# Kernel tuning notes

Hardware: AMD Instinct MI355X
Metric: run time of the kernel (lower is better)

The kernel has to match this reference:

```python
import jax, jax.numpy as jnp
import numpy as np


def _lstm_layer(x, w_ih, w_hh, b_ih, b_hh):
    """Single PyTorch-style LSTM layer (gate order i,f,g,o). x: [B,T,D] -> [B,T,H]."""
    B, T, _ = x.shape
    H = w_hh.shape[1]
    # Precompute input projections for all timesteps (one big GEMM).
    xp = jnp.einsum('btd,gd->btg', x, w_ih) + b_ih + b_hh  # [B,T,4H]

    def step(carry, xt):
        h, c = carry
        gates = xt + h @ w_hh.T  # [B,4H]
        i, f, g, o = jnp.split(gates, 4, axis=-1)
        i = jax.nn.sigmoid(i)
        f = jax.nn.sigmoid(f)
        g = jnp.tanh(g)
        o = jax.nn.sigmoid(o)
        c = f * c + i * g
        h = o * jnp.tanh(c)
        return (h, c), h

    init = (jnp.zeros((B, H), x.dtype), jnp.zeros((B, H), x.dtype))
    _, hs = jax.lax.scan(step, init, jnp.swapaxes(xp, 0, 1))  # hs: [T,B,H]
    return jnp.swapaxes(hs, 0, 1)


def setup_inputs() -> dict:
    key = jax.random.key(0)
    ks = jax.random.split(key, 11)
    B, T, D, H, O = 256, 512, 64, 512, 1
    s_in = 1.0 / np.sqrt(H)
    inp = {
        'x': jax.random.normal(ks[0], (B, T, D), jnp.float32),
        'w_ih_0': jax.random.normal(ks[1], (4 * H, D), jnp.float32) * s_in,
        'w_hh_0': jax.random.normal(ks[2], (4 * H, H), jnp.float32) * s_in,
        'b_ih_0': jax.random.normal(ks[3], (4 * H,), jnp.float32) * s_in,
        'b_hh_0': jax.random.normal(ks[4], (4 * H,), jnp.float32) * s_in,
        'w_ih_1': jax.random.normal(ks[5], (4 * H, H), jnp.float32) * s_in,
        'w_hh_1': jax.random.normal(ks[6], (4 * H, H), jnp.float32) * s_in,
        'b_ih_1': jax.random.normal(ks[7], (4 * H,), jnp.float32) * s_in,
        'b_hh_1': jax.random.normal(ks[8], (4 * H,), jnp.float32) * s_in,
        'fc_w': jax.random.normal(ks[9], (O, H), jnp.float32) * s_in,
        'fc_b': jax.random.normal(ks[10], (O,), jnp.float32) * s_in,
    }
    return inp


def reference(x, w_ih_0, w_hh_0, b_ih_0, b_hh_0,
              w_ih_1, w_hh_1, b_ih_1, b_hh_1, fc_w, fc_b):
    h0 = _lstm_layer(x, w_ih_0, w_hh_0, b_ih_0, b_hh_0)   # [B,T,H]
    h1 = _lstm_layer(h0, w_ih_1, w_hh_1, b_ih_1, b_hh_1)  # [B,T,H]
    # fc on last timestep only
    return h1[:, -1, :] @ fc_w.T + fc_b  # [B,O]
```

## Files before the change

kernel.cpp:

```cpp
#include <hip/hip_runtime.h>


#define BATCH 256
#define SEQ   512
#define DIN   64
#define HID   512

typedef _Float16 f16_t;
typedef __attribute__((ext_vector_type(8))) _Float16 f16x8;
typedef __attribute__((ext_vector_type(4))) float    f32x4;

#define SCOPE_AGT __HIP_MEMORY_SCOPE_AGENT

__device__ inline f16x8 cvt8(const float* __restrict__ p) {
    f16x8 r;
#pragma unroll
    for (int j = 0; j < 8; j++) r[j] = (_Float16)p[j];
    return r;
}

__device__ inline f16x8 cvt8v(f32x4 lo, f32x4 hi) {
    f16x8 r;
#pragma unroll
    for (int j = 0; j < 4; j++) { r[j] = (_Float16)lo[j]; r[4 + j] = (_Float16)hi[j]; }
    return r;
}

__device__ inline f16x8 ldx8(const f16_t* p) {
    const unsigned long long* q = (const unsigned long long*)p;
    unsigned long long a = __hip_atomic_load(q,     __ATOMIC_RELAXED, SCOPE_AGT);
    unsigned long long b = __hip_atomic_load(q + 1, __ATOMIC_RELAXED, SCOPE_AGT);
    union { unsigned long long u[2]; f16x8 v; } c;
    c.u[0] = a; c.u[1] = b;
    return c.v;
}

__device__ inline void sth2a(f16_t* base_even, float h, float hn) {
    union { struct { _Float16 lo, hi; } s; unsigned u; } pk;
    pk.s.lo = (_Float16)h; pk.s.hi = (_Float16)hn;
    __hip_atomic_store((unsigned*)base_even, pk.u, __ATOMIC_RELAXED, SCOPE_AGT);
}

__device__ inline void pollw(const unsigned* p, unsigned need, int lane) {
    for (;;) {
        unsigned v = __hip_atomic_load(p + lane, __ATOMIC_RELAXED, SCOPE_AGT);
        if (__all((int)(v >= need))) break;
        __builtin_amdgcn_s_sleep(1);
    }
}

__device__ inline float sgm(float v) { return 1.f / (1.f + __expf(-v)); }
__device__ inline float th(float v)  { return 1.f - 2.f / (__expf(2.f * v) + 1.f); }

__global__ __launch_bounds__(256, 1) void lstm_pipe(
    const float* __restrict__ x,
    const float* __restrict__ wih0, const float* __restrict__ whh0,
    const float* __restrict__ bih0, const float* __restrict__ bhh0,
    const float* __restrict__ wih1, const float* __restrict__ whh1,
    const float* __restrict__ bih1, const float* __restrict__ bhh1,
    unsigned* __restrict__ f0m, unsigned* __restrict__ f1,
    f16_t* __restrict__ h1buf, f16_t* __restrict__ h0hist)
{
    __shared__ f32x4 red[5][17][64];

    const int tid  = threadIdx.x;
    const int w    = tid >> 6, lane = tid & 63;
    const int quad = lane >> 4, col = lane & 15;
    const int bid  = blockIdx.x;

    if (bid < 128) {
        const int g = bid & 7, s = bid >> 3;
        unsigned* myf = f0m + g * 64;
        const int mym = w & 1, myct = w >> 1;

        f16x8 Wh[32];
#pragma unroll
        for (int i = 0; i < 4; i++) {
            const int k0 = (w * 4 + i) * 32 + quad * 8;
#pragma unroll
            for (int ct = 0; ct < 2; ct++)
#pragma unroll
                for (int nt = 0; nt < 4; nt++) {
                    const int gr = nt * HID + s * 32 + ct * 16 + col;
                    Wh[i * 8 + ct * 4 + nt] = cvt8(whh0 + (size_t)gr * HID + k0);
                }
        }
        f16x8 Wx[8];
        if (w >= 2) {
#pragma unroll
            for (int ct = 0; ct < 2; ct++)
#pragma unroll
                for (int nt = 0; nt < 4; nt++) {
                    const int gr = nt * HID + s * 32 + ct * 16 + col;
                    Wx[ct * 4 + nt] = cvt8(wih0 + (size_t)gr * DIN + (w - 2) * 32 + quad * 8);
                }
        } else {
#pragma unroll
            for (int j = 0; j < 8; j++) Wx[j] = (f16x8)(_Float16)0;
        }
#pragma unroll
        for (int i = 0; i < 32; i++) asm volatile("" : "+v"(Wh[i]));
#pragma unroll
        for (int i = 0; i < 8; i++)  asm volatile("" : "+v"(Wx[i]));

        float bias[4];
#pragma unroll
        for (int nt = 0; nt < 4; nt++) {
            const int gr = nt * HID + s * 32 + myct * 16 + col;
            bias[nt] = bih0[gr] + bhh0[gr];
        }
        float cst[4] = {0, 0, 0, 0};
        unsigned pw0 = 0, pw1 = 0, pw2 = 0, pw3 = 0;

        for (int it = 0; it < SEQ; ++it) {
            asm volatile("" : "+v"(pw0), "+v"(pw1), "+v"(pw2), "+v"(pw3));

            f32x4 xr[4];
            if (w >= 2) {
#pragma unroll
                for (int m = 0; m < 2; m++) {
                    const float* px = x + ((size_t)(g * 32 + m * 16 + col) * SEQ + it) * DIN + (w - 2) * 32 + quad * 8;
                    xr[m * 2]     = *(const f32x4*)px;
                    xr[m * 2 + 1] = *(const f32x4*)(px + 4);
                }
            }
            if (w == 0 && it >= 1) pollw(myf, (unsigned)it, lane);
            __syncthreads();

            f32x4 acc[16];
#pragma unroll
            for (int j = 0; j < 16; j++) acc[j] = (f32x4){0.f, 0.f, 0.f, 0.f};

            if (it > 0) {
                const f16_t* h0b = h0hist + (size_t)(it - 1) * BATCH * HID;
                f16x8 ab[8];
#pragma unroll
                for (int i = 0; i < 4; i++)
#pragma unroll
                    for (int m = 0; m < 2; m++)
                        ab[i * 2 + m] = *(const f16x8*)(h0b + (size_t)(g * 32 + m * 16 + col) * HID
                                                        + (w * 4 + i) * 32 + quad * 8);
#pragma unroll
                for (int i = 0; i < 4; i++)
#pragma unroll
                    for (int m = 0; m < 2; m++)
#pragma unroll
                        for (int ct = 0; ct < 2; ct++)
#pragma unroll
                            for (int nt = 0; nt < 4; nt++)
                                acc[m * 8 + ct * 4 + nt] = __builtin_amdgcn_mfma_f32_16x16x32_f16(
                                    ab[i * 2 + m], Wh[i * 8 + ct * 4 + nt], acc[m * 8 + ct * 4 + nt], 0, 0, 0);
            }
            if (w >= 2) {
#pragma unroll
                for (int m = 0; m < 2; m++) {
                    f16x8 a = cvt8v(xr[m * 2], xr[m * 2 + 1]);
#pragma unroll
                    for (int ct = 0; ct < 2; ct++)
#pragma unroll
                        for (int nt = 0; nt < 4; nt++)
                            acc[m * 8 + ct * 4 + nt] = __builtin_amdgcn_mfma_f32_16x16x32_f16(
                                a, Wx[ct * 4 + nt], acc[m * 8 + ct * 4 + nt], 0, 0, 0);
                }
            }

            if (it + 1 < SEQ) {
                const f16_t* hw = h0hist + (size_t)(it + 1) * BATCH * HID;
                const f16_t* rw = hw + (size_t)(g * 32 + mym * 16 + quad * 4) * HID
                                     + s * 32 + myct * 16 + (col & ~1);
                pw0 = __hip_atomic_load((const unsigned*)(rw),            __ATOMIC_RELAXED, SCOPE_AGT);
                pw1 = __hip_atomic_load((const unsigned*)(rw + HID),      __ATOMIC_RELAXED, SCOPE_AGT);
                pw2 = __hip_atomic_load((const unsigned*)(rw + 2 * HID),  __ATOMIC_RELAXED, SCOPE_AGT);
                pw3 = __hip_atomic_load((const unsigned*)(rw + 3 * HID),  __ATOMIC_RELAXED, SCOPE_AGT);
            }

#pragma unroll
            for (int j = 0; j < 16; j++) red[w][j][lane] = acc[j];
            __syncthreads();

            f32x4 gate[4];
#pragma unroll
            for (int nt = 0; nt < 4; nt++) {
                f32x4 v = red[0][mym * 8 + myct * 4 + nt][lane];
#pragma unroll
                for (int ww = 1; ww < 4; ww++) {
                    f32x4 p = red[ww][mym * 8 + myct * 4 + nt][lane];
#pragma unroll
                    for (int r = 0; r < 4; r++) v[r] += p[r];
                }
                gate[nt] = v;
            }
            f16_t* hout = h0hist + (size_t)it * BATCH * HID;
#pragma unroll
            for (int r = 0; r < 4; r++) {
                float iv = sgm(gate[0][r] + bias[0]), fv = sgm(gate[1][r] + bias[1]);
                float gv = th(gate[2][r] + bias[2]),  ov = sgm(gate[3][r] + bias[3]);
                float c = fv * cst[r] + iv * gv;
                cst[r] = c;
                float h = ov * th(c);
                float hn = __shfl_down(h, 1);
                if ((lane & 1) == 0)
                    sth2a(hout + (size_t)(g * 32 + mym * 16 + quad * 4 + r) * HID + s * 32 + myct * 16 + col, h, hn);
            }
            asm volatile("s_waitcnt vmcnt(0)" ::: "memory");
            if (lane == 0)
                __hip_atomic_store(myf + s * 4 + mym * 2 + myct, (unsigned)(it + 1), __ATOMIC_RELAXED, SCOPE_AGT);
        }
    } else {
        const int idx = bid - 128;
        const int G = idx & 3, s1 = idx >> 2;
        unsigned* myf1 = f1 + G * 32;

        f16x8 Wb[32];
#pragma unroll
        for (int i = 0; i < 8; i++) {
            const int kb = w * 8 + i;
            const int k0 = kb * 32 + quad * 8;
#pragma unroll
            for (int nt = 0; nt < 4; nt++) {
                const int grow = nt * HID + s1 * 16 + col;
                const float* src = (kb < 16) ? (wih1 + (size_t)grow * HID + k0)
                                             : (whh1 + (size_t)grow * HID + (k0 - 512));
                Wb[i * 4 + nt] = cvt8(src);
            }
        }
#pragma unroll
        for (int i = 0; i < 32; i++) asm volatile("" : "+v"(Wb[i]));

        const int d = s1 * 16 + col;
        const float bi = bih1[d] + bhh1[d];
        const float bf = bih1[HID + d] + bhh1[HID + d];
        const float bg = bih1[2 * HID + d] + bhh1[2 * HID + d];
        const float bo = bih1[3 * HID + d] + bhh1[3 * HID + d];
        float cst[4] = {0, 0, 0, 0};

        for (int it = 1; it <= SEQ; ++it) {
            const int t = it - 1;
            if (w == 0) {
                const unsigned* pa = f0m + (2 * G) * 64;
                const unsigned* pb = f0m + (2 * G + 1) * 64;
                const bool chk = (it >= 2);
                for (;;) {
                    unsigned va = __hip_atomic_load(pa + lane, __ATOMIC_RELAXED, SCOPE_AGT);
                    unsigned vb = __hip_atomic_load(pb + lane, __ATOMIC_RELAXED, SCOPE_AGT);
                    unsigned vc = chk ? __hip_atomic_load(myf1 + (lane & 31), __ATOMIC_RELAXED, SCOPE_AGT)
                                      : 0xffffffffu;
                    if (__all((int)((va >= (unsigned)it) & (vb >= (unsigned)it) & (vc >= (unsigned)(it - 1))))) break;
                    __builtin_amdgcn_s_sleep(1);
                }
            }
            __syncthreads();

            f32x4 acc[16];
#pragma unroll
            for (int j = 0; j < 16; j++) acc[j] = (f32x4){0.f, 0.f, 0.f, 0.f};

            const f16_t* h0b = h0hist + (size_t)t * BATCH * HID;
            const f16_t* h1r = h1buf + (size_t)((t - 1) & 1) * BATCH * HID;

            if (w < 2) {
#pragma unroll
                for (int half = 0; half < 2; half++) {
                    f16x8 ab[16];
#pragma unroll
                    for (int i = 0; i < 4; i++)
#pragma unroll
                        for (int mt = 0; mt < 4; mt++)
                            ab[i * 4 + mt] = *(const f16x8*)(h0b + (size_t)(G * 64 + mt * 16 + col) * HID
                                                             + (w * 8 + half * 4 + i) * 32 + quad * 8);
#pragma unroll
                    for (int i = 0; i < 4; i++)
#pragma unroll
                        for (int mt = 0; mt < 4; mt++)
#pragma unroll
                            for (int nt = 0; nt < 4; nt++)
                                acc[mt * 4 + nt] = __builtin_amdgcn_mfma_f32_16x16x32_f16(
                                    ab[i * 4 + mt], Wb[(half * 4 + i) * 4 + nt], acc[mt * 4 + nt], 0, 0, 0);
                }
            } else if (t > 0) {
#pragma unroll
                for (int half = 0; half < 2; half++) {
                    f16x8 ab[16];
#pragma unroll
                    for (int i = 0; i < 4; i++)
#pragma unroll
                        for (int mt = 0; mt < 4; mt++)
                            ab[i * 4 + mt] = ldx8(h1r + (size_t)(G * 64 + mt * 16 + col) * HID
                                                  + (w * 8 + half * 4 + i - 16) * 32 + quad * 8);
#pragma unroll
                    for (int i = 0; i < 4; i++)
#pragma unroll
                        for (int mt = 0; mt < 4; mt++)
#pragma unroll
                            for (int nt = 0; nt < 4; nt++)
                                acc[mt * 4 + nt] = __builtin_amdgcn_mfma_f32_16x16x32_f16(
                                    ab[i * 4 + mt], Wb[(half * 4 + i) * 4 + nt], acc[mt * 4 + nt], 0, 0, 0);
                }
            }
#pragma unroll
            for (int j = 0; j < 16; j++) red[w][j][lane] = acc[j];
            __syncthreads();

            f32x4 gate[4];
#pragma unroll
            for (int nt = 0; nt < 4; nt++) {
                f32x4 v = red[0][w * 4 + nt][lane];
#pragma unroll
                for (int ww = 1; ww < 4; ww++) {
                    f32x4 p = red[ww][w * 4 + nt][lane];
#pragma unroll
                    for (int r = 0; r < 4; r++) v[r] += p[r];
                }
                gate[nt] = v;
            }
            f16_t* hout = h1buf + (size_t)(t & 1) * BATCH * HID;
#pragma unroll
            for (int r = 0; r < 4; r++) {
                float iv = sgm(gate[0][r] + bi), fv = sgm(gate[1][r] + bf);
                float gv = th(gate[2][r] + bg),  ov = sgm(gate[3][r] + bo);
                float c = fv * cst[r] + iv * gv;
                cst[r] = c;
                float h = ov * th(c);
                float hn = __shfl_down(h, 1);
                if ((lane & 1) == 0)
                    sth2a(hout + (size_t)(G * 64 + w * 16 + quad * 4 + r) * HID + s1 * 16 + col, h, hn);
            }
            __syncthreads();
            if (tid == 0)
                __hip_atomic_store(myf1 + s1, (unsigned)it, __ATOMIC_RELAXED, SCOPE_AGT);
        }
    }
}

__global__ void fc_k(const f16_t* __restrict__ h1buf, const float* __restrict__ fcw,
                     const float* __restrict__ fcb, float* __restrict__ out)
{
    const int b = blockIdx.x, lane = threadIdx.x;
    const f16_t* hp = h1buf + ((size_t)(BATCH + b)) * HID;
    float sum = 0.f;
#pragma unroll
    for (int j = 0; j < 8; j++) {
        const int k = lane * 8 + j;
        sum += (float)hp[k] * fcw[k];
    }
#pragma unroll
    for (int off = 32; off; off >>= 1) sum += __shfl_down(sum, off);
    if (lane == 0) out[b] = sum + fcb[0];
}

extern "C" void kernel_launch(void* const* d_in, const int* in_sizes, int n_in,
                              void* d_out, int out_size, void* d_ws, size_t ws_size,
                              hipStream_t stream)
{
    const float* x    = (const float*)d_in[0];
    const float* wih0 = (const float*)d_in[1];
    const float* whh0 = (const float*)d_in[2];
    const float* bih0 = (const float*)d_in[3];
    const float* bhh0 = (const float*)d_in[4];
    const float* wih1 = (const float*)d_in[5];
    const float* whh1 = (const float*)d_in[6];
    const float* bih1 = (const float*)d_in[7];
    const float* bhh1 = (const float*)d_in[8];
    const float* fcw  = (const float*)d_in[9];
    const float* fcb  = (const float*)d_in[10];
    float* out = (float*)d_out;

    unsigned char* ws = (unsigned char*)d_ws;
    unsigned* f0m = (unsigned*)ws;
    unsigned* f1  = (unsigned*)(ws + 2048);
    f16_t* h1buf  = (f16_t*)(ws + 4096);
    f16_t* h0hist = (f16_t*)(ws + 4096 + 2 * BATCH * HID * sizeof(f16_t));

    hipMemsetAsync(ws, 0, 4096, stream);
    lstm_pipe<<<dim3(256), dim3(256), 0, stream>>>(x, wih0, whh0, bih0, bhh0,
                                                   wih1, whh1, bih1, bhh1,
                                                   f0m, f1, h1buf, h0hist);
    fc_k<<<dim3(BATCH), dim3(64), 0, stream>>>(h1buf, fcw, fcb, out);
}
```

Baseline: 4.470 ms.

## Store hidden states in MFMA-fragment layout with LDS-staged 8-byte stores

Changes the global layout of the h0 history and h1 ping-pong buffers so each wavefront's MFMA A-operand fragment is a contiguous 64-lane x 8-half block. Loads become fully coalesced 16-byte reads per lane. Hidden outputs are staged in shared memory and written as one 8-byte atomic store per lane, replacing scattered 4-byte paired stores. The prefetch touch of the next step drops from four loads to one. The fc kernel is updated to read the new layout.

Measured after the change: 6.348 ms. 1.42x slower.

```diff
diff --git a/kernel.cpp b/kernel.cpp
--- a/kernel.cpp
+++ b/kernel.cpp
@@ -5,6 +5,8 @@
 #define SEQ   512
 #define DIN   64
 #define HID   512
+
+#define HSTEP 131072
 
 typedef _Float16 f16_t;
 typedef __attribute__((ext_vector_type(8))) _Float16 f16x8;
@@ -35,12 +37,6 @@
     return c.v;
 }
 
-__device__ inline void sth2a(f16_t* base_even, float h, float hn) {
-    union { struct { _Float16 lo, hi; } s; unsigned u; } pk;
-    pk.s.lo = (_Float16)h; pk.s.hi = (_Float16)hn;
-    __hip_atomic_store((unsigned*)base_even, pk.u, __ATOMIC_RELAXED, SCOPE_AGT);
-}
-
 __device__ inline void pollw(const unsigned* p, unsigned need, int lane) {
     for (;;) {
         unsigned v = __hip_atomic_load(p + lane, __ATOMIC_RELAXED, SCOPE_AGT);
@@ -59,9 +55,10 @@
     const float* __restrict__ wih1, const float* __restrict__ whh1,
     const float* __restrict__ bih1, const float* __restrict__ bhh1,
     unsigned* __restrict__ f0m, unsigned* __restrict__ f1,
-    f16_t* __restrict__ h1buf, f16_t* __restrict__ h0hist)
+    f16_t* __restrict__ h1f, f16_t* __restrict__ h0hist)
 {
     __shared__ f32x4 red[5][17][64];
+    __shared__ f16_t stg[4][32][8];
 
     const int tid  = threadIdx.x;
     const int w    = tid >> 6, lane = tid & 63;
@@ -110,10 +107,12 @@
             bias[nt] = bih0[gr] + bhh0[gr];
         }
         float cst[4] = {0, 0, 0, 0};
-        unsigned pw0 = 0, pw1 = 0, pw2 = 0, pw3 = 0;
+        unsigned pw0 = 0;
+
+        const size_t wbase = ((size_t)(s * 16 + g * 2 + mym) * 64 + myct * 32) * 8;
 
         for (int it = 0; it < SEQ; ++it) {
-            asm volatile("" : "+v"(pw0), "+v"(pw1), "+v"(pw2), "+v"(pw3));
+            asm volatile("" : "+v"(pw0));
 
             f32x4 xr[4];
             if (w >= 2) {
@@ -132,14 +131,14 @@
             for (int j = 0; j < 16; j++) acc[j] = (f32x4){0.f, 0.f, 0.f, 0.f};
 
             if (it > 0) {
-                const f16_t* h0b = h0hist + (size_t)(it - 1) * BATCH * HID;
+                const f16_t* h0b = h0hist + (size_t)(it - 1) * HSTEP;
                 f16x8 ab[8];
 #pragma unroll
                 for (int i = 0; i < 4; i++)
 #pragma unroll
                     for (int m = 0; m < 2; m++)
-                        ab[i * 2 + m] = *(const f16x8*)(h0b + (size_t)(g * 32 + m * 16 + col) * HID
-                                                        + (w * 4 + i) * 32 + quad * 8);
+                        ab[i * 2 + m] = *(const f16x8*)(h0b +
+                            (((size_t)((w * 4 + i) * 16 + g * 2 + m)) * 64 + lane) * 8);
 #pragma unroll
                 for (int i = 0; i < 4; i++)
 #pragma unroll
@@ -164,14 +163,9 @@
                 }
             }
 
-            if (it + 1 < SEQ) {
-                const f16_t* hw = h0hist + (size_t)(it + 1) * BATCH * HID;
-                const f16_t* rw = hw + (size_t)(g * 32 + mym * 16 + quad * 4) * HID
-                                     + s * 32 + myct * 16 + (col & ~1);
-                pw0 = __hip_atomic_load((const unsigned*)(rw),            __ATOMIC_RELAXED, SCOPE_AGT);
-                pw1 = __hip_atomic_load((const unsigned*)(rw + HID),      __ATOMIC_RELAXED, SCOPE_AGT);
-                pw2 = __hip_atomic_load((const unsigned*)(rw + 2 * HID),  __ATOMIC_RELAXED, SCOPE_AGT);
-                pw3 = __hip_atomic_load((const unsigned*)(rw + 3 * HID),  __ATOMIC_RELAXED, SCOPE_AGT);
+            if (it + 1 < SEQ && lane < 4) {
+                const f16_t* rw = h0hist + (size_t)(it + 1) * HSTEP + wbase + (size_t)lane * 64;
+                pw0 = __hip_atomic_load((const unsigned*)rw, __ATOMIC_RELAXED, SCOPE_AGT);
             }
 
 #pragma unroll
@@ -190,7 +184,6 @@
                 }
                 gate[nt] = v;
             }
-            f16_t* hout = h0hist + (size_t)it * BATCH * HID;
 #pragma unroll
             for (int r = 0; r < 4; r++) {
                 float iv = sgm(gate[0][r] + bias[0]), fv = sgm(gate[1][r] + bias[1]);
@@ -198,9 +191,13 @@
                 float c = fv * cst[r] + iv * gv;
                 cst[r] = c;
                 float h = ov * th(c);
-                float hn = __shfl_down(h, 1);
-                if ((lane & 1) == 0)
-                    sth2a(hout + (size_t)(g * 32 + mym * 16 + quad * 4 + r) * HID + s * 32 + myct * 16 + col, h, hn);
+                stg[w][(col >> 3) * 16 + quad * 4 + r][col & 7] = (f16_t)h;
+            }
+            asm volatile("s_waitcnt lgkmcnt(0)" ::: "memory");
+            {
+                unsigned long long v = *(const unsigned long long*)&stg[w][lane >> 1][(lane & 1) * 4];
+                f16_t* dst = h0hist + (size_t)it * HSTEP + wbase + (size_t)lane * 4;
+                __hip_atomic_store((unsigned long long*)dst, v, __ATOMIC_RELAXED, SCOPE_AGT);
             }
             asm volatile("s_waitcnt vmcnt(0)" ::: "memory");
             if (lane == 0)
@@ -233,6 +230,8 @@
         const float bg = bih1[2 * HID + d] + bhh1[2 * HID + d];
         const float bo = bih1[3 * HID + d] + bhh1[3 * HID + d];
         float cst[4] = {0, 0, 0, 0};
+
+        const size_t wbase1 = ((size_t)((s1 >> 1) * 16 + G * 4 + w) * 64 + (s1 & 1) * 32) * 8;
 
         for (int it = 1; it <= SEQ; ++it) {
             const int t = it - 1;
@@ -255,8 +254,8 @@
 #pragma unroll
             for (int j = 0; j < 16; j++) acc[j] = (f32x4){0.f, 0.f, 0.f, 0.f};
 
-            const f16_t* h0b = h0hist + (size_t)t * BATCH * HID;
-            const f16_t* h1r = h1buf + (size_t)((t - 1) & 1) * BATCH * HID;
+            const f16_t* h0b = h0hist + (size_t)t * HSTEP;
+            const f16_t* h1r = h1f + (size_t)((t - 1) & 1) * HSTEP;
 
             if (w < 2) {
 #pragma unroll
@@ -266,8 +265,8 @@
                     for (int i = 0; i < 4; i++)
 #pragma unroll
                         for (int mt = 0; mt < 4; mt++)
-                            ab[i * 4 + mt] = *(const f16x8*)(h0b + (size_t)(G * 64 + mt * 16 + col) * HID
-                                                             + (w * 8 + half * 4 + i) * 32 + quad * 8);
+                            ab[i * 4 + mt] = *(const f16x8*)(h0b +
+                                (((size_t)((w * 8 + half * 4 + i) * 16 + G * 4 + mt)) * 64 + lane) * 8);
 #pragma unroll
                     for (int i = 0; i < 4; i++)
 #pragma unroll
@@ -285,8 +284,8 @@
                     for (int i = 0; i < 4; i++)
 #pragma unroll
                         for (int mt = 0; mt < 4; mt++)
-                            ab[i * 4 + mt] = ldx8(h1r + (size_t)(G * 64 + mt * 16 + col) * HID
-                                                  + (w * 8 + half * 4 + i - 16) * 32 + quad * 8);
+                            ab[i * 4 + mt] = ldx8(h1r +
+                                (((size_t)((w * 8 + half * 4 + i - 16) * 16 + G * 4 + mt)) * 64 + lane) * 8);
 #pragma unroll
                     for (int i = 0; i < 4; i++)
 #pragma unroll
@@ -313,7 +312,6 @@
                 }
                 gate[nt] = v;
             }
-            f16_t* hout = h1buf + (size_t)(t & 1) * BATCH * HID;
 #pragma unroll
             for (int r = 0; r < 4; r++) {
                 float iv = sgm(gate[0][r] + bi), fv = sgm(gate[1][r] + bf);
@@ -321,9 +319,13 @@
                 float c = fv * cst[r] + iv * gv;
                 cst[r] = c;
                 float h = ov * th(c);
-                float hn = __shfl_down(h, 1);
-                if ((lane & 1) == 0)
-                    sth2a(hout + (size_t)(G * 64 + w * 16 + quad * 4 + r) * HID + s1 * 16 + col, h, hn);
+                stg[w][(col >> 3) * 16 + quad * 4 + r][col & 7] = (f16_t)h;
+            }
+            asm volatile("s_waitcnt lgkmcnt(0)" ::: "memory");
+            {
+                unsigned long long v = *(const unsigned long long*)&stg[w][lane >> 1][(lane & 1) * 4];
+                f16_t* dst = h1f + (size_t)(t & 1) * HSTEP + wbase1 + (size_t)lane * 4;
+                __hip_atomic_store((unsigned long long*)dst, v, __ATOMIC_RELAXED, SCOPE_AGT);
             }
             __syncthreads();
             if (tid == 0)
@@ -332,17 +334,16 @@
     }
 }
 
-__global__ void fc_k(const f16_t* __restrict__ h1buf, const float* __restrict__ fcw,
+__global__ void fc_k(const f16_t* __restrict__ h1f, const float* __restrict__ fcw,
                      const float* __restrict__ fcb, float* __restrict__ out)
 {
     const int b = blockIdx.x, lane = threadIdx.x;
-    const f16_t* hp = h1buf + ((size_t)(BATCH + b)) * HID;
+    const size_t idx = (size_t)HSTEP +
+        (((size_t)((lane >> 2) * 16 + (b >> 4))) * 64 + ((lane & 3) * 16 + (b & 15))) * 8;
+    const f16x8 hv = *(const f16x8*)(h1f + idx);
     float sum = 0.f;
 #pragma unroll
-    for (int j = 0; j < 8; j++) {
-        const int k = lane * 8 + j;
-        sum += (float)hp[k] * fcw[k];
-    }
+    for (int j = 0; j < 8; j++) sum += (float)hv[j] * fcw[lane * 8 + j];
 #pragma unroll
     for (int off = 32; off; off >>= 1) sum += __shfl_down(sum, off);
     if (lane == 0) out[b] = sum + fcb[0];
@@ -368,12 +369,12 @@
     unsigned char* ws = (unsigned char*)d_ws;
     unsigned* f0m = (unsigned*)ws;
     unsigned* f1  = (unsigned*)(ws + 2048);
-    f16_t* h1buf  = (f16_t*)(ws + 4096);
-    f16_t* h0hist = (f16_t*)(ws + 4096 + 2 * BATCH * HID * sizeof(f16_t));
+    f16_t* h1f    = (f16_t*)(ws + 4096);
+    f16_t* h0hist = (f16_t*)(ws + 4096 + (size_t)2 * HSTEP * sizeof(f16_t));
 
     hipMemsetAsync(ws, 0, 4096, stream);
     lstm_pipe<<<dim3(256), dim3(256), 0, stream>>>(x, wih0, whh0, bih0, bhh0,
                                                    wih1, whh1, bih1, bhh1,
-                                                   f0m, f1, h1buf, h0hist);
-    fc_k<<<dim3(BATCH), dim3(64), 0, stream>>>(h1buf, fcw, fcb, out);
-}
+                                                   f0m, f1, h1f, h0hist);
+    fc_k<<<dim3(BATCH), dim3(64), 0, stream>>>(h1f, fcw, fcb, out);
+}
```
